# Optimization experiments

Measured on AMD Instinct MI355X. Metric: run time of the kernel, lower is better.

The kernel has to match this reference:

```python
import jax, jax.numpy as jnp
import numpy as np

EOS_TOKEN = 1


def setup_inputs() -> dict:
    key = jax.random.key(0)
    ks = jax.random.split(key, 14)
    B, S, H = 512, 128, 512
    SV, IV = 2000, 8192
    s = 1.0 / np.sqrt(H)

    def u(k, shape):
        return jax.random.uniform(k, shape, jnp.float32, -s, s)

    return {
        "goal_batch": jax.random.randint(ks[0], (B, S), 0, IV),
        "stem_batch": jax.random.randint(ks[1], (B,), 0, SV),
        # nn.Embedding default init: N(0,1)
        "stem_emb": jax.random.normal(ks[2], (SV, H), jnp.float32),
        "word_emb": jax.random.normal(ks[3], (IV, H), jnp.float32),
        # nn.GRU weights (1 layer): weight_ih_l0 [3H,H], weight_hh_l0 [3H,H]
        "W_ih": u(ks[4], (3 * H, H)),
        "W_hh": u(ks[5], (3 * H, H)),
        "b_ih": u(ks[6], (3 * H,)),
        "b_hh": u(ks[7], (3 * H,)),
        # EncoderDNN(hidden, hidden, 1, num_layers=2): in_layer, one hidden layer, out_layer
        "in_W": u(ks[8], (H, H)),
        "in_b": u(ks[9], (H,)),
        "l0_W": u(ks[10], (H, H)),
        "l0_b": u(ks[11], (H,)),
        "out_W": u(ks[12], (1, H)),
        "out_b": u(ks[13], (1,)),
    }


def _gru_step(h, xt, W_ih, W_hh, b_ih, b_hh):
    # PyTorch GRU cell semantics
    gi = xt @ W_ih.T + b_ih  # [B, 3H]
    gh = h @ W_hh.T + b_hh   # [B, 3H]
    ir, iz, in_ = jnp.split(gi, 3, axis=-1)
    hr, hz, hn = jnp.split(gh, 3, axis=-1)
    r = jax.nn.sigmoid(ir + hr)
    z = jax.nn.sigmoid(iz + hz)
    n = jnp.tanh(in_ + r * hn)
    return (1.0 - z) * n + z * h


def _likelyhood(v, in_W, in_b, l0_W, l0_b, out_W, out_b):
    # EncoderDNN applied to F.relu(token_out): in -> relu -> layer0 -> relu -> out
    v = jax.nn.relu(v)
    v = jax.nn.relu(v @ in_W.T + in_b)
    v = jax.nn.relu(v @ l0_W.T + l0_b)
    return v @ out_W.T + out_b  # [..., 1]


def reference(goal_batch, stem_batch, stem_emb, word_emb, W_ih, W_hh, b_ih, b_hh,
              in_W, in_b, l0_W, l0_b, out_W, out_b):
    B = goal_batch.shape[0]
    h0 = stem_emb[stem_batch]                      # [B, H] initial hidden from stem
    xs = jax.nn.relu(word_emb[goal_batch])         # [B, S, H]
    xs = jnp.swapaxes(xs, 0, 1)                    # [S, B, H]

    def step(h, xt):
        hn = _gru_step(h, xt, W_ih, W_hh, b_ih, b_hh)
        return hn, hn

    h_last, hs = jax.lax.scan(step, h0, xs)        # hs: [S, B, H]

    eos_x = jnp.broadcast_to(jax.nn.relu(word_emb[EOS_TOKEN]), (B, word_emb.shape[1]))
    h_final = _gru_step(h_last, eos_x, W_ih, W_hh, b_ih, b_hh)  # [B, H]

    seq_like = _likelyhood(hs, in_W, in_b, l0_W, l0_b, out_W, out_b)[..., 0].T  # [B, S]
    fin_like = _likelyhood(h_final, in_W, in_b, l0_W, l0_b, out_W, out_b)       # [B, 1]

    logits = jnp.concatenate([fin_like, seq_like], axis=1)  # EOS likelihood prepended
    return jax.nn.log_softmax(logits, axis=1)               # [B, S+1]
```

## Files before the change

### kernel.cpp

```cpp
#include <hip/hip_runtime.h>
#include <math.h>

#define B_    512
#define S_    128
#define H_    512
#define H3_   1536
#define IV_   8192
#define OUTC_ 129
#define CHUNK_ 16512
#define EOS_  1

__global__ __launch_bounds__(256)
void build_h0(const int* __restrict__ stem_batch,
              const float* __restrict__ stem_emb,
              float* __restrict__ h0) {
    int i = blockIdx.x * blockDim.x + threadIdx.x;
    int b = i >> 7;
    int c = (i & 127) << 2;
    int row = stem_batch[b];
    float4 v = *(const float4*)&stem_emb[(size_t)row * H_ + c];
    *(float4*)&h0[(size_t)b * H_ + c] = v;
}

template<bool RELU_IN, bool RELU_OUT>
__global__ __launch_bounds__(256)
void gemm_nt(const float* __restrict__ A, const float* __restrict__ W,
             const float* __restrict__ bias, float* __restrict__ C,
             int M, int N, int K) {
    __shared__ float As[64][33];
    __shared__ float Ws[64][33];
    const int tid = threadIdx.x;
    const int bm = blockIdx.y * 64;
    const int bn = blockIdx.x * 64;
    const int tx = tid & 15;
    const int ty = tid >> 4;
    const int lr = tid >> 3;
    const int lc = (tid & 7) << 2;

    float acc[4][4] = {};

    for (int k0 = 0; k0 < K; k0 += 32) {
        float4 a0 = *(const float4*)&A[(size_t)(bm + lr)      * K + k0 + lc];
        float4 a1 = *(const float4*)&A[(size_t)(bm + lr + 32) * K + k0 + lc];
        float4 w0 = *(const float4*)&W[(size_t)(bn + lr)      * K + k0 + lc];
        float4 w1 = *(const float4*)&W[(size_t)(bn + lr + 32) * K + k0 + lc];
        if (RELU_IN) {
            a0.x = fmaxf(a0.x, 0.f); a0.y = fmaxf(a0.y, 0.f);
            a0.z = fmaxf(a0.z, 0.f); a0.w = fmaxf(a0.w, 0.f);
            a1.x = fmaxf(a1.x, 0.f); a1.y = fmaxf(a1.y, 0.f);
            a1.z = fmaxf(a1.z, 0.f); a1.w = fmaxf(a1.w, 0.f);
        }
        __syncthreads();
        *(float4*)&As[lr][lc]      = a0;
        *(float4*)&As[lr + 32][lc] = a1;
        *(float4*)&Ws[lr][lc]      = w0;
        *(float4*)&Ws[lr + 32][lc] = w1;
        __syncthreads();
        #pragma unroll
        for (int kk = 0; kk < 32; ++kk) {
            float av[4], wv[4];
            #pragma unroll
            for (int i = 0; i < 4; ++i) av[i] = As[ty * 4 + i][kk];
            #pragma unroll
            for (int j = 0; j < 4; ++j) wv[j] = Ws[tx * 4 + j][kk];
            #pragma unroll
            for (int i = 0; i < 4; ++i)
                #pragma unroll
                for (int j = 0; j < 4; ++j)
                    acc[i][j] += av[i] * wv[j];
        }
    }

    #pragma unroll
    for (int i = 0; i < 4; ++i) {
        int m = bm + ty * 4 + i;
        #pragma unroll
        for (int j = 0; j < 4; ++j) {
            int n = bn + tx * 4 + j;
            float c = acc[i][j] + bias[n];
            if (RELU_OUT) c = fmaxf(c, 0.f);
            C[(size_t)m * N + n] = c;
        }
    }
}

__global__ __launch_bounds__(256)
void gru_step(const float* __restrict__ h_in, float* __restrict__ h_out,
              const float* __restrict__ GW, const int* __restrict__ goal,
              int t, const float* __restrict__ W_hh,
              const float* __restrict__ b_hh) {
    __shared__ float Hs[32][65];
    __shared__ float Wr[32][65];
    __shared__ float Wz[32][65];
    __shared__ float Wn[32][65];
    const int tid = threadIdx.x;
    const int bm = blockIdx.y * 32;
    const int bn = blockIdx.x * 32;
    const int tx = tid & 15;
    const int ty = tid >> 4;
    const int lr = tid >> 4;
    const int lc = (tid & 15) << 2;

    float ar[2][2] = {}, az[2][2] = {}, an[2][2] = {};

    for (int k0 = 0; k0 < H_; k0 += 64) {
        float4 h0v = *(const float4*)&h_in[(size_t)(bm + lr)      * H_ + k0 + lc];
        float4 h1v = *(const float4*)&h_in[(size_t)(bm + lr + 16) * H_ + k0 + lc];
        float4 r0 = *(const float4*)&W_hh[(size_t)(bn + lr)              * H_ + k0 + lc];
        float4 r1 = *(const float4*)&W_hh[(size_t)(bn + lr + 16)         * H_ + k0 + lc];
        float4 z0 = *(const float4*)&W_hh[(size_t)(512 + bn + lr)        * H_ + k0 + lc];
        float4 z1 = *(const float4*)&W_hh[(size_t)(512 + bn + lr + 16)   * H_ + k0 + lc];
        float4 n0 = *(const float4*)&W_hh[(size_t)(1024 + bn + lr)       * H_ + k0 + lc];
        float4 n1 = *(const float4*)&W_hh[(size_t)(1024 + bn + lr + 16)  * H_ + k0 + lc];
        __syncthreads();
        *(float4*)&Hs[lr][lc]      = h0v;
        *(float4*)&Hs[lr + 16][lc] = h1v;
        *(float4*)&Wr[lr][lc]      = r0;
        *(float4*)&Wr[lr + 16][lc] = r1;
        *(float4*)&Wz[lr][lc]      = z0;
        *(float4*)&Wz[lr + 16][lc] = z1;
        *(float4*)&Wn[lr][lc]      = n0;
        *(float4*)&Wn[lr + 16][lc] = n1;
        __syncthreads();
        #pragma unroll
        for (int kk = 0; kk < 64; ++kk) {
            float hm0 = Hs[ty * 2][kk],     hm1 = Hs[ty * 2 + 1][kk];
            float wr0 = Wr[tx * 2][kk],     wr1 = Wr[tx * 2 + 1][kk];
            float wz0 = Wz[tx * 2][kk],     wz1 = Wz[tx * 2 + 1][kk];
            float wn0 = Wn[tx * 2][kk],     wn1 = Wn[tx * 2 + 1][kk];
            ar[0][0] += hm0 * wr0; ar[0][1] += hm0 * wr1;
            ar[1][0] += hm1 * wr0; ar[1][1] += hm1 * wr1;
            az[0][0] += hm0 * wz0; az[0][1] += hm0 * wz1;
            az[1][0] += hm1 * wz0; az[1][1] += hm1 * wz1;
            an[0][0] += hm0 * wn0; an[0][1] += hm0 * wn1;
            an[1][0] += hm1 * wn0; an[1][1] += hm1 * wn1;
        }
    }

    #pragma unroll
    for (int i = 0; i < 2; ++i) {
        int b = bm + ty * 2 + i;
        int grow = (t < S_) ? goal[(size_t)b * S_ + t] : EOS_;
        const float* gw = GW + (size_t)grow * H3_;
        #pragma unroll
        for (int jj = 0; jj < 2; ++jj) {
            int j = bn + tx * 2 + jj;
            float gir = gw[j];
            float giz = gw[j + 512];
            float gin = gw[j + 1024];
            float ghr = ar[i][jj] + b_hh[j];
            float ghz = az[i][jj] + b_hh[j + 512];
            float ghn = an[i][jj] + b_hh[j + 1024];
            float r = 1.f / (1.f + expf(-(gir + ghr)));
            float z = 1.f / (1.f + expf(-(giz + ghz)));
            float n = tanhf(gin + r * ghn);
            float hp = h_in[(size_t)b * H_ + j];
            h_out[(size_t)b * H_ + j] = (1.f - z) * n + z * hp;
        }
    }
}

__global__ __launch_bounds__(256)
void gemv_out(const float* __restrict__ Y2, const float* __restrict__ outW,
              const float* __restrict__ outb, float* __restrict__ out,
              int row0) {
    int wave = threadIdx.x >> 6;
    int lane = threadIdx.x & 63;
    int row = blockIdx.x * 4 + wave;
    const float* y = Y2 + (size_t)row * H_;
    float4 v0 = *(const float4*)&y[lane * 4];
    float4 v1 = *(const float4*)&y[256 + lane * 4];
    float4 w0 = *(const float4*)&outW[lane * 4];
    float4 w1 = *(const float4*)&outW[256 + lane * 4];
    float s = v0.x * w0.x + v0.y * w0.y + v0.z * w0.z + v0.w * w0.w
            + v1.x * w1.x + v1.y * w1.y + v1.z * w1.z + v1.w * w1.w;
    #pragma unroll
    for (int off = 32; off > 0; off >>= 1) s += __shfl_down(s, off);
    if (lane == 0) {
        int r = row0 + row;
        int t = r / B_;
        int b = r - t * B_;
        int pos = (t == S_) ? 0 : t + 1;
        out[(size_t)b * OUTC_ + pos] = s + outb[0];
    }
}

__global__ __launch_bounds__(64)
void logsoftmax_rows(float* __restrict__ out) {
    int b = blockIdx.x;
    int lane = threadIdx.x;
    float* row = out + (size_t)b * OUTC_;
    float x0 = row[lane];
    float x1 = row[lane + 64];
    float x2 = (lane == 0) ? row[128] : -INFINITY;
    float m = fmaxf(fmaxf(x0, x1), x2);
    #pragma unroll
    for (int off = 32; off > 0; off >>= 1) m = fmaxf(m, __shfl_xor(m, off));
    float s = expf(x0 - m) + expf(x1 - m) + ((lane == 0) ? expf(x2 - m) : 0.f);
    #pragma unroll
    for (int off = 32; off > 0; off >>= 1) s += __shfl_xor(s, off);
    float ls = m + logf(s);
    row[lane] = x0 - ls;
    row[lane + 64] = x1 - ls;
    if (lane == 0) row[128] = x2 - ls;
}

extern "C" void kernel_launch(void* const* d_in, const int* in_sizes, int n_in,
                              void* d_out, int out_size, void* d_ws, size_t ws_size,
                              hipStream_t stream) {
    const int*   goal     = (const int*)d_in[0];
    const int*   stem     = (const int*)d_in[1];
    const float* stem_emb = (const float*)d_in[2];
    const float* word_emb = (const float*)d_in[3];
    const float* W_ih     = (const float*)d_in[4];
    const float* W_hh     = (const float*)d_in[5];
    const float* b_ih     = (const float*)d_in[6];
    const float* b_hh     = (const float*)d_in[7];
    const float* in_W     = (const float*)d_in[8];
    const float* in_b     = (const float*)d_in[9];
    const float* l0_W     = (const float*)d_in[10];
    const float* l0_b     = (const float*)d_in[11];
    const float* out_W    = (const float*)d_in[12];
    const float* out_b    = (const float*)d_in[13];
    float* out = (float*)d_out;

    float* GW = (float*)d_ws;
    float* HS = GW + (size_t)IV_ * H3_;
    float* Y1 = HS + (size_t)(S_ + 2) * B_ * H_;
    float* Y2 = Y1 + (size_t)CHUNK_ * H_;

    build_h0<<<(B_ * H_ / 4) / 256, 256, 0, stream>>>(stem, stem_emb, HS);

    gemm_nt<true, false><<<dim3(H3_ / 64, IV_ / 64), 256, 0, stream>>>(
        word_emb, W_ih, b_ih, GW, IV_, H3_, H_);

    for (int t = 0; t <= S_; ++t) {
        gru_step<<<dim3(H_ / 32, B_ / 32), 256, 0, stream>>>(
            HS + (size_t)t * B_ * H_, HS + (size_t)(t + 1) * B_ * H_,
            GW, goal, t, W_hh, b_hh);
    }

    for (int c = 0; c < 4; ++c) {
        const float* hsrc = HS + (size_t)B_ * H_ + (size_t)c * CHUNK_ * H_;
        gemm_nt<true, true><<<dim3(H_ / 64, CHUNK_ / 64), 256, 0, stream>>>(
            hsrc, in_W, in_b, Y1, CHUNK_, H_, H_);
        gemm_nt<false, true><<<dim3(H_ / 64, CHUNK_ / 64), 256, 0, stream>>>(
            Y1, l0_W, l0_b, Y2, CHUNK_, H_, H_);
        gemv_out<<<CHUNK_ / 4, 256, 0, stream>>>(Y2, out_W, out_b, out, c * CHUNK_);
    }

    logsoftmax_rows<<<B_, 64, 0, stream>>>(out);
}
```

Baseline: 6.377 ms.

## Use split-bf16 MFMA GEMMs for GRU recurrence and MLP layers

```diff
diff --git a/kernel.cpp b/kernel.cpp
--- a/kernel.cpp
+++ b/kernel.cpp
@@ -7,163 +7,250 @@
 #define H3_   1536
 #define IV_   8192
 #define OUTC_ 129
-#define CHUNK_ 16512
+#define CHUNK_ 11008
+#define NCHUNK_ 6
 #define EOS_  1
 
-__global__ __launch_bounds__(256)
-void build_h0(const int* __restrict__ stem_batch,
-              const float* __restrict__ stem_emb,
-              float* __restrict__ h0) {
-    int i = blockIdx.x * blockDim.x + threadIdx.x;
+typedef __attribute__((ext_vector_type(8))) short  bf16x8;
+typedef __attribute__((ext_vector_type(4))) float  f32x4;
+
+__device__ inline unsigned short f2bf(float f) {
+    union { float f; unsigned u; } x; x.f = f;
+    unsigned r = x.u + 0x7FFF + ((x.u >> 16) & 1);
+    return (unsigned short)(r >> 16);
+}
+__device__ inline float bf2f(unsigned short b) {
+    union { unsigned u; float f; } x; x.u = ((unsigned)b) << 16;
+    return x.f;
+}
+
+template<bool RELU>
+__global__ __launch_bounds__(256)
+void split_f32(const float* __restrict__ src, unsigned short* __restrict__ hi,
+               unsigned short* __restrict__ lo, int n4) {
+    int i = blockIdx.x * 256 + threadIdx.x;
+    if (i >= n4) return;
+    float4 v = *(const float4*)&src[(size_t)i * 4];
+    float a[4] = {v.x, v.y, v.z, v.w};
+    size_t off = (size_t)i * 4;
+    #pragma unroll
+    for (int q = 0; q < 4; ++q) {
+        float f = RELU ? fmaxf(a[q], 0.f) : a[q];
+        unsigned short h = f2bf(f);
+        hi[off + q] = h;
+        lo[off + q] = f2bf(f - bf2f(h));
+    }
+}
+
+__global__ __launch_bounds__(256)
+void build_h0_split(const int* __restrict__ stem, const float* __restrict__ stem_emb,
+                    unsigned short* __restrict__ Hh, unsigned short* __restrict__ Hl) {
+    int i = blockIdx.x * 256 + threadIdx.x;
     int b = i >> 7;
     int c = (i & 127) << 2;
-    int row = stem_batch[b];
-    float4 v = *(const float4*)&stem_emb[(size_t)row * H_ + c];
-    *(float4*)&h0[(size_t)b * H_ + c] = v;
-}
-
-template<bool RELU_IN, bool RELU_OUT>
-__global__ __launch_bounds__(256)
-void gemm_nt(const float* __restrict__ A, const float* __restrict__ W,
-             const float* __restrict__ bias, float* __restrict__ C,
-             int M, int N, int K) {
-    __shared__ float As[64][33];
-    __shared__ float Ws[64][33];
+    float4 v = *(const float4*)&stem_emb[(size_t)stem[b] * H_ + c];
+    float a[4] = {v.x, v.y, v.z, v.w};
+    size_t off = (size_t)b * H_ + c;
+    #pragma unroll
+    for (int q = 0; q < 4; ++q) {
+        unsigned short h = f2bf(a[q]);
+        Hh[off + q] = h;
+        Hl[off + q] = f2bf(a[q] - bf2f(h));
+    }
+}
+
+template<int OUT_MODE, bool RELU_OUT>
+__global__ __launch_bounds__(256)
+void gemm_split(const unsigned short* __restrict__ Ah, const unsigned short* __restrict__ Al,
+                const unsigned short* __restrict__ Wh, const unsigned short* __restrict__ Wl,
+                const float* __restrict__ bias,
+                float* __restrict__ Cf, unsigned short* __restrict__ Chi,
+                unsigned short* __restrict__ Clo, int M, int N, int K) {
+    __shared__ unsigned short As[128][72];
+    __shared__ unsigned short Ws[128][72];
     const int tid = threadIdx.x;
-    const int bm = blockIdx.y * 64;
-    const int bn = blockIdx.x * 64;
-    const int tx = tid & 15;
-    const int ty = tid >> 4;
-    const int lr = tid >> 3;
-    const int lc = (tid & 7) << 2;
-
-    float acc[4][4] = {};
-
-    for (int k0 = 0; k0 < K; k0 += 32) {
-        float4 a0 = *(const float4*)&A[(size_t)(bm + lr)      * K + k0 + lc];
-        float4 a1 = *(const float4*)&A[(size_t)(bm + lr + 32) * K + k0 + lc];
-        float4 w0 = *(const float4*)&W[(size_t)(bn + lr)      * K + k0 + lc];
-        float4 w1 = *(const float4*)&W[(size_t)(bn + lr + 32) * K + k0 + lc];
-        if (RELU_IN) {
-            a0.x = fmaxf(a0.x, 0.f); a0.y = fmaxf(a0.y, 0.f);
-            a0.z = fmaxf(a0.z, 0.f); a0.w = fmaxf(a0.w, 0.f);
-            a1.x = fmaxf(a1.x, 0.f); a1.y = fmaxf(a1.y, 0.f);
-            a1.z = fmaxf(a1.z, 0.f); a1.w = fmaxf(a1.w, 0.f);
+    const int bm = blockIdx.y * 128, bn = blockIdx.x * 128;
+    const int wid = tid >> 6, lane = tid & 63;
+    const int wm = (wid >> 1) * 64, wn = (wid & 1) * 64;
+    const int lr = lane & 15, kg = (lane >> 4) * 8;
+
+    f32x4 acc[4][4];
+    #pragma unroll
+    for (int i = 0; i < 4; ++i)
+        #pragma unroll
+        for (int j = 0; j < 4; ++j) acc[i][j] = f32x4{0.f, 0.f, 0.f, 0.f};
+
+    for (int ph = 0; ph < 3; ++ph) {
+        const unsigned short* Ap = (ph == 1) ? Al : Ah;
+        const unsigned short* Wp = (ph == 2) ? Wl : Wh;
+        for (int k0 = 0; k0 < K; k0 += 64) {
+            int4 av[4], wv[4];
+            #pragma unroll
+            for (int s = 0; s < 4; ++s) {
+                int seg = s * 256 + tid;
+                int row = seg >> 3, c8 = (seg & 7) * 8;
+                av[s] = *(const int4*)&Ap[(size_t)(bm + row) * K + k0 + c8];
+                wv[s] = *(const int4*)&Wp[(size_t)(bn + row) * K + k0 + c8];
+            }
+            __syncthreads();
+            #pragma unroll
+            for (int s = 0; s < 4; ++s) {
+                int seg = s * 256 + tid;
+                int row = seg >> 3, c8 = (seg & 7) * 8;
+                *(int4*)&As[row][c8] = av[s];
+                *(int4*)&Ws[row][c8] = wv[s];
+            }
+            __syncthreads();
+            #pragma unroll
+            for (int ks = 0; ks < 2; ++ks) {
+                bf16x8 af[4], bfr[4];
+                #pragma unroll
+                for (int i = 0; i < 4; ++i)
+                    af[i] = *(const bf16x8*)&As[wm + i * 16 + lr][ks * 32 + kg];
+                #pragma unroll
+                for (int j = 0; j < 4; ++j)
+                    bfr[j] = *(const bf16x8*)&Ws[wn + j * 16 + lr][ks * 32 + kg];
+                #pragma unroll
+                for (int i = 0; i < 4; ++i)
+                    #pragma unroll
+                    for (int j = 0; j < 4; ++j)
+                        acc[i][j] = __builtin_amdgcn_mfma_f32_16x16x32_bf16(
+                            af[i], bfr[j], acc[i][j], 0, 0, 0);
+            }
         }
-        __syncthreads();
-        *(float4*)&As[lr][lc]      = a0;
-        *(float4*)&As[lr + 32][lc] = a1;
-        *(float4*)&Ws[lr][lc]      = w0;
-        *(float4*)&Ws[lr + 32][lc] = w1;
-        __syncthreads();
-        #pragma unroll
-        for (int kk = 0; kk < 32; ++kk) {
-            float av[4], wv[4];
-            #pragma unroll
-            for (int i = 0; i < 4; ++i) av[i] = As[ty * 4 + i][kk];
-            #pragma unroll
-            for (int j = 0; j < 4; ++j) wv[j] = Ws[tx * 4 + j][kk];
-            #pragma unroll
-            for (int i = 0; i < 4; ++i)
-                #pragma unroll
-                for (int j = 0; j < 4; ++j)
-                    acc[i][j] += av[i] * wv[j];
-        }
-    }
-
+    }
+
+    const int r0 = (lane >> 4) * 4, cn = lane & 15;
     #pragma unroll
     for (int i = 0; i < 4; ++i) {
-        int m = bm + ty * 4 + i;
         #pragma unroll
         for (int j = 0; j < 4; ++j) {
-            int n = bn + tx * 4 + j;
-            float c = acc[i][j] + bias[n];
-            if (RELU_OUT) c = fmaxf(c, 0.f);
-            C[(size_t)m * N + n] = c;
+            int colg = bn + wn + j * 16 + cn;
+            float bv = bias[colg];
+            #pragma unroll
+            for (int rg = 0; rg < 4; ++rg) {
+                int rowg = bm + wm + i * 16 + r0 + rg;
+                float v = acc[i][j][rg] + bv;
+                if (RELU_OUT) v = fmaxf(v, 0.f);
+                size_t off = (size_t)rowg * N + colg;
+                if (OUT_MODE == 0) {
+                    Cf[off] = v;
+                } else {
+                    unsigned short h = f2bf(v);
+                    Chi[off] = h;
+                    Clo[off] = f2bf(v - bf2f(h));
+                }
+            }
         }
     }
 }
 
 __global__ __launch_bounds__(256)
-void gru_step(const float* __restrict__ h_in, float* __restrict__ h_out,
-              const float* __restrict__ GW, const int* __restrict__ goal,
-              int t, const float* __restrict__ W_hh,
-              const float* __restrict__ b_hh) {
-    __shared__ float Hs[32][65];
-    __shared__ float Wr[32][65];
-    __shared__ float Wz[32][65];
-    __shared__ float Wn[32][65];
+void gru_step_mfma(const unsigned short* __restrict__ Hih, const unsigned short* __restrict__ Hil,
+                   unsigned short* __restrict__ Hoh, unsigned short* __restrict__ Hol,
+                   unsigned short* __restrict__ RHh, unsigned short* __restrict__ RHl,
+                   const unsigned short* __restrict__ Wh, const unsigned short* __restrict__ Wl,
+                   const float* __restrict__ GW, const float* __restrict__ b_hh,
+                   const int* __restrict__ goal, int t) {
+    __shared__ unsigned short As[128][72];
+    __shared__ unsigned short Bs[96][72];
     const int tid = threadIdx.x;
-    const int bm = blockIdx.y * 32;
     const int bn = blockIdx.x * 32;
-    const int tx = tid & 15;
-    const int ty = tid >> 4;
-    const int lr = tid >> 4;
-    const int lc = (tid & 15) << 2;
-
-    float ar[2][2] = {}, az[2][2] = {}, an[2][2] = {};
-
-    for (int k0 = 0; k0 < H_; k0 += 64) {
-        float4 h0v = *(const float4*)&h_in[(size_t)(bm + lr)      * H_ + k0 + lc];
-        float4 h1v = *(const float4*)&h_in[(size_t)(bm + lr + 16) * H_ + k0 + lc];
-        float4 r0 = *(const float4*)&W_hh[(size_t)(bn + lr)              * H_ + k0 + lc];
-        float4 r1 = *(const float4*)&W_hh[(size_t)(bn + lr + 16)         * H_ + k0 + lc];
-        float4 z0 = *(const float4*)&W_hh[(size_t)(512 + bn + lr)        * H_ + k0 + lc];
-        float4 z1 = *(const float4*)&W_hh[(size_t)(512 + bn + lr + 16)   * H_ + k0 + lc];
-        float4 n0 = *(const float4*)&W_hh[(size_t)(1024 + bn + lr)       * H_ + k0 + lc];
-        float4 n1 = *(const float4*)&W_hh[(size_t)(1024 + bn + lr + 16)  * H_ + k0 + lc];
-        __syncthreads();
-        *(float4*)&Hs[lr][lc]      = h0v;
-        *(float4*)&Hs[lr + 16][lc] = h1v;
-        *(float4*)&Wr[lr][lc]      = r0;
-        *(float4*)&Wr[lr + 16][lc] = r1;
-        *(float4*)&Wz[lr][lc]      = z0;
-        *(float4*)&Wz[lr + 16][lc] = z1;
-        *(float4*)&Wn[lr][lc]      = n0;
-        *(float4*)&Wn[lr + 16][lc] = n1;
-        __syncthreads();
+    const int bm = blockIdx.y * 128;
+    const int w = tid >> 6, lane = tid & 63;
+    const int lr = lane & 15, kg = (lane >> 4) * 8;
+
+    f32x4 acc[2][6];
+    #pragma unroll
+    for (int i = 0; i < 2; ++i)
         #pragma unroll
-        for (int kk = 0; kk < 64; ++kk) {
-            float hm0 = Hs[ty * 2][kk],     hm1 = Hs[ty * 2 + 1][kk];
-            float wr0 = Wr[tx * 2][kk],     wr1 = Wr[tx * 2 + 1][kk];
-            float wz0 = Wz[tx * 2][kk],     wz1 = Wz[tx * 2 + 1][kk];
-            float wn0 = Wn[tx * 2][kk],     wn1 = Wn[tx * 2 + 1][kk];
-            ar[0][0] += hm0 * wr0; ar[0][1] += hm0 * wr1;
-            ar[1][0] += hm1 * wr0; ar[1][1] += hm1 * wr1;
-            az[0][0] += hm0 * wz0; az[0][1] += hm0 * wz1;
-            az[1][0] += hm1 * wz0; az[1][1] += hm1 * wz1;
-            an[0][0] += hm0 * wn0; an[0][1] += hm0 * wn1;
-            an[1][0] += hm1 * wn0; an[1][1] += hm1 * wn1;
+        for (int f = 0; f < 6; ++f) acc[i][f] = f32x4{0.f, 0.f, 0.f, 0.f};
+
+    for (int ph = 0; ph < 3; ++ph) {
+        const unsigned short* Ap = (ph == 1) ? Hil : Hih;
+        const unsigned short* Wp = (ph == 2) ? Wl : Wh;
+        for (int k0 = 0; k0 < H_; k0 += 64) {
+            int4 av[4], wv[3];
+            #pragma unroll
+            for (int s = 0; s < 4; ++s) {
+                int seg = s * 256 + tid;
+                int row = seg >> 3, c8 = (seg & 7) * 8;
+                av[s] = *(const int4*)&Ap[(size_t)(bm + row) * H_ + k0 + c8];
+            }
+            #pragma unroll
+            for (int s = 0; s < 3; ++s) {
+                int seg = s * 256 + tid;
+                int beta = seg >> 3, c8 = (seg & 7) * 8;
+                int wrow = ((beta >> 5) << 9) + bn + (beta & 31);
+                wv[s] = *(const int4*)&Wp[(size_t)wrow * H_ + k0 + c8];
+            }
+            __syncthreads();
+            #pragma unroll
+            for (int s = 0; s < 4; ++s) {
+                int seg = s * 256 + tid;
+                *(int4*)&As[seg >> 3][(seg & 7) * 8] = av[s];
+            }
+            #pragma unroll
+            for (int s = 0; s < 3; ++s) {
+                int seg = s * 256 + tid;
+                *(int4*)&Bs[seg >> 3][(seg & 7) * 8] = wv[s];
+            }
+            __syncthreads();
+            #pragma unroll
+            for (int ks = 0; ks < 2; ++ks) {
+                bf16x8 af[2], bfr[6];
+                #pragma unroll
+                for (int i = 0; i < 2; ++i)
+                    af[i] = *(const bf16x8*)&As[w * 32 + i * 16 + lr][ks * 32 + kg];
+                #pragma unroll
+                for (int f = 0; f < 6; ++f)
+                    bfr[f] = *(const bf16x8*)&Bs[f * 16 + lr][ks * 32 + kg];
+                #pragma unroll
+                for (int i = 0; i < 2; ++i)
+                    #pragma unroll
+                    for (int f = 0; f < 6; ++f)
+                        acc[i][f] = __builtin_amdgcn_mfma_f32_16x16x32_bf16(
+                            af[i], bfr[f], acc[i][f], 0, 0, 0);
+            }
         }
     }
 
+    const int r0 = (lane >> 4) * 4, cn = lane & 15;
     #pragma unroll
     for (int i = 0; i < 2; ++i) {
-        int b = bm + ty * 2 + i;
-        int grow = (t < S_) ? goal[(size_t)b * S_ + t] : EOS_;
-        const float* gw = GW + (size_t)grow * H3_;
         #pragma unroll
-        for (int jj = 0; jj < 2; ++jj) {
-            int j = bn + tx * 2 + jj;
-            float gir = gw[j];
-            float giz = gw[j + 512];
-            float gin = gw[j + 1024];
-            float ghr = ar[i][jj] + b_hh[j];
-            float ghz = az[i][jj] + b_hh[j + 512];
-            float ghn = an[i][jj] + b_hh[j + 1024];
-            float r = 1.f / (1.f + expf(-(gir + ghr)));
-            float z = 1.f / (1.f + expf(-(giz + ghz)));
-            float n = tanhf(gin + r * ghn);
-            float hp = h_in[(size_t)b * H_ + j];
-            h_out[(size_t)b * H_ + j] = (1.f - z) * n + z * hp;
+        for (int rg = 0; rg < 4; ++rg) {
+            int b = bm + w * 32 + i * 16 + r0 + rg;
+            int tok = (t < S_) ? goal[(size_t)b * S_ + t] : EOS_;
+            const float* gw = GW + (size_t)tok * H3_;
+            #pragma unroll
+            for (int jf = 0; jf < 2; ++jf) {
+                int j = bn + jf * 16 + cn;
+                float rp = acc[i][jf][rg]     + b_hh[j];
+                float zp = acc[i][2 + jf][rg] + b_hh[512 + j];
+                float hn = acc[i][4 + jf][rg] + b_hh[1024 + j];
+                float r = 1.f / (1.f + expf(-(gw[j] + rp)));
+                float z = 1.f / (1.f + expf(-(gw[512 + j] + zp)));
+                float n = tanhf(gw[1024 + j] + r * hn);
+                size_t off = (size_t)b * H_ + j;
+                float hp = bf2f(Hih[off]) + bf2f(Hil[off]);
+                float hv = (1.f - z) * n + z * hp;
+                unsigned short hh = f2bf(hv);
+                Hoh[off] = hh;
+                Hol[off] = f2bf(hv - bf2f(hh));
+                float rv = fmaxf(hv, 0.f);
+                unsigned short rh = f2bf(rv);
+                size_t roff = ((size_t)t * B_ + b) * H_ + j;
+                RHh[roff] = rh;
+                RHl[roff] = f2bf(rv - bf2f(rh));
+            }
         }
     }
 }
 
 __global__ __launch_bounds__(256)
 void gemv_out(const float* __restrict__ Y2, const float* __restrict__ outW,
-              const float* __restrict__ outb, float* __restrict__ out,
-              int row0) {
+              const float* __restrict__ outb, float* __restrict__ out, int row0) {
     int wave = threadIdx.x >> 6;
     int lane = threadIdx.x & 63;
     int row = blockIdx.x * 4 + wave;
@@ -224,28 +311,56 @@
     const float* out_b    = (const float*)d_in[13];
     float* out = (float*)d_out;
 
-    float* GW = (float*)d_ws;
-    float* HS = GW + (size_t)IV_ * H3_;
-    float* Y1 = HS + (size_t)(S_ + 2) * B_ * H_;
-    float* Y2 = Y1 + (size_t)CHUNK_ * H_;
-
-    build_h0<<<(B_ * H_ / 4) / 256, 256, 0, stream>>>(stem, stem_emb, HS);
-
-    gemm_nt<true, false><<<dim3(H3_ / 64, IV_ / 64), 256, 0, stream>>>(
-        word_emb, W_ih, b_ih, GW, IV_, H3_, H_);
+    char* base = (char*)d_ws;
+    auto alloc = [&](size_t bytes) -> char* {
+        char* p = base; base += (bytes + 255) & ~(size_t)255; return p;
+    };
+    float* GW            = (float*)alloc((size_t)IV_ * H3_ * 4);
+    unsigned short* RHh  = (unsigned short*)alloc((size_t)(S_ + 1) * B_ * H_ * 2);
+    unsigned short* RHl  = (unsigned short*)alloc((size_t)(S_ + 1) * B_ * H_ * 2);
+    unsigned short* WHHh = (unsigned short*)alloc((size_t)H3_ * H_ * 2);
+    unsigned short* WHHl = (unsigned short*)alloc((size_t)H3_ * H_ * 2);
+    unsigned short* INWh = (unsigned short*)alloc((size_t)H_ * H_ * 2);
+    unsigned short* INWl = (unsigned short*)alloc((size_t)H_ * H_ * 2);
+    unsigned short* L0Wh = (unsigned short*)alloc((size_t)H_ * H_ * 2);
+    unsigned short* L0Wl = (unsigned short*)alloc((size_t)H_ * H_ * 2);
+    unsigned short* Hh[2], *Hl[2];
+    Hh[0] = (unsigned short*)alloc((size_t)B_ * H_ * 2);
+    Hl[0] = (unsigned short*)alloc((size_t)B_ * H_ * 2);
+    Hh[1] = (unsigned short*)alloc((size_t)B_ * H_ * 2);
+    Hl[1] = (unsigned short*)alloc((size_t)B_ * H_ * 2);
+    char* uni = alloc((size_t)CHUNK_ * H_ * (2 + 2 + 4));
+    unsigned short* RWEh = (unsigned short*)uni;
+    unsigned short* RWEl = RWEh + (size_t)IV_ * H_;
+    unsigned short* WIHh = RWEl + (size_t)IV_ * H_;
+    unsigned short* WIHl = WIHh + (size_t)H3_ * H_;
+    unsigned short* Y1h  = (unsigned short*)uni;
+    unsigned short* Y1l  = Y1h + (size_t)CHUNK_ * H_;
+    float* Y2            = (float*)(Y1l + (size_t)CHUNK_ * H_);
+
+    split_f32<true ><<<(IV_ * H_ / 4) / 256, 256, 0, stream>>>(word_emb, RWEh, RWEl, IV_ * H_ / 4);
+    split_f32<false><<<(H3_ * H_ / 4) / 256, 256, 0, stream>>>(W_ih, WIHh, WIHl, H3_ * H_ / 4);
+    split_f32<false><<<(H3_ * H_ / 4) / 256, 256, 0, stream>>>(W_hh, WHHh, WHHl, H3_ * H_ / 4);
+    split_f32<false><<<(H_ * H_ / 4) / 256, 256, 0, stream>>>(in_W, INWh, INWl, H_ * H_ / 4);
+    split_f32<false><<<(H_ * H_ / 4) / 256, 256, 0, stream>>>(l0_W, L0Wh, L0Wl, H_ * H_ / 4);
+
+    build_h0_split<<<(B_ * H_ / 4) / 256, 256, 0, stream>>>(stem, stem_emb, Hh[0], Hl[0]);
+
+    gemm_split<0, false><<<dim3(H3_ / 128, IV_ / 128), 256, 0, stream>>>(
+        RWEh, RWEl, WIHh, WIHl, b_ih, GW, nullptr, nullptr, IV_, H3_, H_);
 
     for (int t = 0; t <= S_; ++t) {
-        gru_step<<<dim3(H_ / 32, B_ / 32), 256, 0, stream>>>(
-            HS + (size_t)t * B_ * H_, HS + (size_t)(t + 1) * B_ * H_,
-            GW, goal, t, W_hh, b_hh);
-    }
-
-    for (int c = 0; c < 4; ++c) {
-        const float* hsrc = HS + (size_t)B_ * H_ + (size_t)c * CHUNK_ * H_;
-        gemm_nt<true, true><<<dim3(H_ / 64, CHUNK_ / 64), 256, 0, stream>>>(
-            hsrc, in_W, in_b, Y1, CHUNK_, H_, H_);
-        gemm_nt<false, true><<<dim3(H_ / 64, CHUNK_ / 64), 256, 0, stream>>>(
-            Y1, l0_W, l0_b, Y2, CHUNK_, H_, H_);
+        int a = t & 1, o = (t + 1) & 1;
+        gru_step_mfma<<<dim3(H_ / 32, B_ / 128), 256, 0, stream>>>(
+            Hh[a], Hl[a], Hh[o], Hl[o], RHh, RHl, WHHh, WHHl, GW, b_hh, goal, t);
+    }
+
+    for (int c = 0; c < NCHUNK_; ++c) {
+        size_t ro = (size_t)c * CHUNK_ * H_;
+        gemm_split<1, true><<<dim3(H_ / 128, CHUNK_ / 128), 256, 0, stream>>>(
+            RHh + ro, RHl + ro, INWh, INWl, in_b, nullptr, Y1h, Y1l, CHUNK_, H_, H_);
+        gemm_split<0, true><<<dim3(H_ / 128, CHUNK_ / 128), 256, 0, stream>>>(
+            Y1h, Y1l, L0Wh, L0Wl, l0_b, Y2, nullptr, nullptr, CHUNK_, H_, H_);
         gemv_out<<<CHUNK_ / 4, 256, 0, stream>>>(Y2, out_W, out_b, out, c * CHUNK_);
     }
 
```

Result: slower. 11.87 ms (+86.2%).
